# Performance work log

Hardware: AMD Instinct MI355X
Metric: run time of the kernel (lower is better)

Reference implementation:

```python
import math
import jax, jax.numpy as jnp
import numpy as np

E = 300
VOCAB = 50000
NUM_CLASSES = 34
ATTN_H = 150
B, S = 64, 2048


def setup_inputs() -> dict:
    key = jax.random.key(0)
    k1, k2, k3, k4, k5 = jax.random.split(key, 5)
    return {
        "input_x": jax.random.randint(k1, (B, S), 0, VOCAB, dtype=jnp.int32),
        "embedding": jax.random.normal(k2, (VOCAB, E), dtype=jnp.float32),
        "query": jax.random.normal(k3, (1, E), dtype=jnp.float32) * 0.1,
        "W_attention": jax.random.normal(k4, (E, ATTN_H), dtype=jnp.float32) * (1.0 / math.sqrt(E)),
        "W_out": jax.random.normal(k5, (2 * E, NUM_CLASSES), dtype=jnp.float32) * (1.0 / math.sqrt(2 * E)),
        "b": jnp.full((NUM_CLASSES,), 0.1, dtype=jnp.float32),
    }


def reference(input_x, embedding, query, W_attention, W_out, b):
    # Embedding lookup: [B, S, E]
    kv = embedding[input_x]
    scale = 1.0 / math.sqrt(E)
    # Stage 1: single learned query attends over all tokens
    s1 = jnp.einsum('e,bse->bs', query[0], kv) * scale          # [B, S]
    a1 = jax.nn.softmax(s1, axis=-1)
    h1 = jnp.einsum('bs,bse->be', a1, kv)                        # [B, E]
    # Stage 2: project h1 and keys through W_attention (no sqrt scaling in original)
    q2 = h1 @ W_attention                                        # [B, 150]
    k2 = jnp.einsum('bse,eh->bsh', kv, W_attention)              # [B, S, 150]
    s2 = jnp.einsum('bh,bsh->bs', q2, k2)                        # [B, S]
    a2 = jax.nn.softmax(s2, axis=-1)
    h2 = jnp.einsum('bs,bse->be', a2, kv)                        # [B, E]
    h = jnp.concatenate([h1, h2], axis=-1)                       # [B, 2E]
    # Dropout with keep_prob=1.0 (eval) is identity
    scores = h @ W_out + b                                       # [B, num_classes]
    return scores
```

## Files before the change

### kernel.cpp

```cpp
#include <hip/hip_runtime.h>
#include <math.h>

#define B_  64
#define S_  2048
#define E_  300
#define H_  150
#define C_  34
#define CHUNK 128
#define NCHUNK (S_ / CHUNK)
#define WAVES 4

__global__ __launch_bounds__(256, 4) void attn_pass(
    const int* __restrict__ x, const float* __restrict__ emb,
    const float* __restrict__ qmat, int q_stride, float scale,
    float* __restrict__ h_part, float* __restrict__ m_part,
    float* __restrict__ l_part)
{
    const int b     = blockIdx.y;
    const int chunk = blockIdx.x;
    const int tid   = threadIdx.x;
    const int w     = tid >> 6;
    const int lane  = tid & 63;

    const float4* qp = (const float4*)(qmat + (size_t)b * q_stride);
    float4 q0 = qp[lane];
    float4 q1 = make_float4(0.f, 0.f, 0.f, 0.f);
    if (lane < 11) q1 = qp[64 + lane];
    q0.x *= scale; q0.y *= scale; q0.z *= scale; q0.w *= scale;
    q1.x *= scale; q1.y *= scale; q1.z *= scale; q1.w *= scale;

    const int base = b * S_ + chunk * CHUNK;
    int myidx = 0;
    if (lane < 32) myidx = x[base + w + 4 * lane];

    float  m = -INFINITY, l = 0.f;
    float4 a0 = make_float4(0.f, 0.f, 0.f, 0.f);
    float4 a1 = make_float4(0.f, 0.f, 0.f, 0.f);

    for (int g = 0; g < 8; ++g) {
        float4 r0[4], r1[4];
        #pragma unroll
        for (int t = 0; t < 4; ++t) {
            const int row = __shfl(myidx, 4 * g + t);
            const float4* rp = (const float4*)(emb + (size_t)row * E_);
            r0[t] = rp[lane];
            r1[t] = make_float4(0.f, 0.f, 0.f, 0.f);
            if (lane < 11) r1[t] = rp[64 + lane];
        }
        float d[4];
        #pragma unroll
        for (int t = 0; t < 4; ++t)
            d[t] = q0.x * r0[t].x + q0.y * r0[t].y + q0.z * r0[t].z + q0.w * r0[t].w
                 + q1.x * r1[t].x + q1.y * r1[t].y + q1.z * r1[t].z + q1.w * r1[t].w;
        #pragma unroll
        for (int off = 32; off > 0; off >>= 1) {
            #pragma unroll
            for (int t = 0; t < 4; ++t) d[t] += __shfl_xor(d[t], off);
        }
        const float gm = fmaxf(fmaxf(d[0], d[1]), fmaxf(d[2], d[3]));
        const float mn = fmaxf(m, gm);
        const float c  = __expf(m - mn);
        const float p0 = __expf(d[0] - mn), p1 = __expf(d[1] - mn);
        const float p2 = __expf(d[2] - mn), p3 = __expf(d[3] - mn);
        l = l * c + ((p0 + p1) + (p2 + p3));
        a0.x = a0.x * c + p0 * r0[0].x + p1 * r0[1].x + p2 * r0[2].x + p3 * r0[3].x;
        a0.y = a0.y * c + p0 * r0[0].y + p1 * r0[1].y + p2 * r0[2].y + p3 * r0[3].y;
        a0.z = a0.z * c + p0 * r0[0].z + p1 * r0[1].z + p2 * r0[2].z + p3 * r0[3].z;
        a0.w = a0.w * c + p0 * r0[0].w + p1 * r0[1].w + p2 * r0[2].w + p3 * r0[3].w;
        a1.x = a1.x * c + p0 * r1[0].x + p1 * r1[1].x + p2 * r1[2].x + p3 * r1[3].x;
        a1.y = a1.y * c + p0 * r1[0].y + p1 * r1[1].y + p2 * r1[2].y + p3 * r1[3].y;
        a1.z = a1.z * c + p0 * r1[0].z + p1 * r1[1].z + p2 * r1[2].z + p3 * r1[3].z;
        a1.w = a1.w * c + p0 * r1[0].w + p1 * r1[1].w + p2 * r1[2].w + p3 * r1[3].w;
        m = mn;
    }

    __shared__ float sm[WAVES], sl[WAVES];
    __shared__ __align__(16) float sacc[WAVES][304];
    ((float4*)sacc[w])[lane] = a0;
    if (lane < 11) ((float4*)sacc[w])[64 + lane] = a1;
    if (lane == 0) { sm[w] = m; sl[w] = l; }
    __syncthreads();

    const float mb = fmaxf(fmaxf(sm[0], sm[1]), fmaxf(sm[2], sm[3]));
    const int pi = b * NCHUNK + chunk;
    for (int j = tid; j < E_; j += 256) {
        float h = 0.f;
        #pragma unroll
        for (int c = 0; c < WAVES; ++c)
            h += __expf(sm[c] - mb) * sacc[c][j];
        h_part[(size_t)pi * E_ + j] = h;
    }
    if (tid == 0) {
        float lb = 0.f;
        #pragma unroll
        for (int c = 0; c < WAVES; ++c) lb += __expf(sm[c] - mb) * sl[c];
        m_part[pi] = mb; l_part[pi] = lb;
    }
}

__global__ __launch_bounds__(320) void combine_qv(
    const float* __restrict__ h_part, const float* __restrict__ m_part,
    const float* __restrict__ l_part, const float* __restrict__ W,
    float* __restrict__ h1out, float* __restrict__ v2out)
{
    const int b = blockIdx.x, tid = threadIdx.x;
    __shared__ float sm[NCHUNK], sl[NCHUNK], sh[E_], sq[H_];
    if (tid < NCHUNK) { sm[tid] = m_part[b * NCHUNK + tid];
                        sl[tid] = l_part[b * NCHUNK + tid]; }
    __syncthreads();
    if (tid < E_) {
        float M = -INFINITY;
        #pragma unroll
        for (int c = 0; c < NCHUNK; ++c) M = fmaxf(M, sm[c]);
        float L = 0.f, h = 0.f;
        #pragma unroll
        for (int c = 0; c < NCHUNK; ++c) {
            const float wc = __expf(sm[c] - M);
            L += wc * sl[c];
            h += wc * h_part[((size_t)b * NCHUNK + c) * E_ + tid];
        }
        const float v = h / L;
        sh[tid] = v;
        h1out[b * E_ + tid] = v;
    }
    __syncthreads();
    if (tid < H_) {
        float acc = 0.f;
        for (int e = 0; e < E_; ++e) acc += sh[e] * W[e * H_ + tid];
        sq[tid] = acc;
    }
    __syncthreads();
    if (tid < E_) {
        float acc = 0.f;
        const float* wr = W + (size_t)tid * H_;
        for (int h = 0; h < H_; ++h) acc += sq[h] * wr[h];
        v2out[b * E_ + tid] = acc;
    }
}

__global__ __launch_bounds__(320) void combine_scores(
    const float* __restrict__ h_part, const float* __restrict__ m_part,
    const float* __restrict__ l_part, const float* __restrict__ h1,
    const float* __restrict__ Wout, const float* __restrict__ bias,
    float* __restrict__ out)
{
    const int b = blockIdx.x, tid = threadIdx.x;
    const int w = tid >> 6, lane = tid & 63;
    __shared__ float sm[NCHUNK], sl[NCHUNK];
    __shared__ float hh[2 * E_];
    if (tid < NCHUNK) { sm[tid] = m_part[b * NCHUNK + tid];
                        sl[tid] = l_part[b * NCHUNK + tid]; }
    if (tid < E_) hh[tid] = h1[b * E_ + tid];
    __syncthreads();
    if (tid < E_) {
        float M = -INFINITY;
        #pragma unroll
        for (int c = 0; c < NCHUNK; ++c) M = fmaxf(M, sm[c]);
        float L = 0.f, h = 0.f;
        #pragma unroll
        for (int c = 0; c < NCHUNK; ++c) {
            const float wc = __expf(sm[c] - M);
            L += wc * sl[c];
            h += wc * h_part[((size_t)b * NCHUNK + c) * E_ + tid];
        }
        hh[E_ + tid] = h / L;
    }
    __syncthreads();
    for (int c = w; c < C_; c += 5) {
        float p = 0.f;
        for (int e = lane; e < 2 * E_; e += 64)
            p += hh[e] * Wout[(size_t)e * C_ + c];
        #pragma unroll
        for (int off = 32; off > 0; off >>= 1) p += __shfl_xor(p, off);
        if (lane == 0) out[b * C_ + c] = p + bias[c];
    }
}

extern "C" void kernel_launch(void* const* d_in, const int* in_sizes, int n_in,
                              void* d_out, int out_size, void* d_ws, size_t ws_size,
                              hipStream_t stream) {
    const int*   x     = (const int*)  d_in[0];
    const float* emb   = (const float*)d_in[1];
    const float* query = (const float*)d_in[2];
    const float* Watt  = (const float*)d_in[3];
    const float* Wout  = (const float*)d_in[4];
    const float* bias  = (const float*)d_in[5];
    float* out = (float*)d_out;

    float* ws     = (float*)d_ws;
    float* h_part = ws;
    float* m_part = h_part + (size_t)B_ * NCHUNK * E_;
    float* l_part = m_part + B_ * NCHUNK;
    float* h1     = l_part + B_ * NCHUNK;
    float* v2     = h1 + B_ * E_;

    const float scale1 = 1.0f / sqrtf((float)E_);
    dim3 grid(NCHUNK, B_), blk(256);

    attn_pass<<<grid, blk, 0, stream>>>(x, emb, query, 0, scale1,
                                        h_part, m_part, l_part);
    combine_qv<<<B_, 320, 0, stream>>>(h_part, m_part, l_part, Watt, h1, v2);
    attn_pass<<<grid, blk, 0, stream>>>(x, emb, v2, E_, 1.0f,
                                        h_part, m_part, l_part);
    combine_scores<<<B_, 320, 0, stream>>>(h_part, m_part, l_part, h1,
                                           Wout, bias, out);
}
```

Before: 169.9 us.

## Fuse four kernel launches into one cooperative kernel with grid syncs

Replaces the four separate launches (two attention passes and two combine kernels) with a single cooperative kernel that uses grid-wide syncs between stages. Only chunk 0 of each batch row does the combine and projection work. This is meant to remove launch overhead and inter-kernel gaps. In exchange, the grid of 1024 blocks must be co-resident, the combine stages run on few blocks while others idle at the barrier, and grid.sync has its own cost. A fallback to the old launches is kept if the cooperative launch fails.

```diff
diff --git a/kernel.cpp b/kernel.cpp
--- a/kernel.cpp
+++ b/kernel.cpp
@@ -1,5 +1,8 @@
 #include <hip/hip_runtime.h>
+#include <hip/hip_cooperative_groups.h>
 #include <math.h>
+
+namespace cg = cooperative_groups;
 
 #define B_  64
 #define S_  2048
@@ -10,17 +13,15 @@
 #define NCHUNK (S_ / CHUNK)
 #define WAVES 4
 
-__global__ __launch_bounds__(256, 4) void attn_pass(
+__device__ __forceinline__ void attn_chunk(
     const int* __restrict__ x, const float* __restrict__ emb,
     const float* __restrict__ qmat, int q_stride, float scale,
     float* __restrict__ h_part, float* __restrict__ m_part,
-    float* __restrict__ l_part)
-{
-    const int b     = blockIdx.y;
-    const int chunk = blockIdx.x;
-    const int tid   = threadIdx.x;
-    const int w     = tid >> 6;
-    const int lane  = tid & 63;
+    float* __restrict__ l_part, int b, int chunk, int tid,
+    float* sm, float* sl, float (*sacc)[304])
+{
+    const int w    = tid >> 6;
+    const int lane = tid & 63;
 
     const float4* qp = (const float4*)(qmat + (size_t)b * q_stride);
     float4 q0 = qp[lane];
@@ -74,8 +75,6 @@
         m = mn;
     }
 
-    __shared__ float sm[WAVES], sl[WAVES];
-    __shared__ __align__(16) float sacc[WAVES][304];
     ((float4*)sacc[w])[lane] = a0;
     if (lane < 11) ((float4*)sacc[w])[64 + lane] = a1;
     if (lane == 0) { sm[w] = m; sl[w] = l; }
@@ -86,16 +85,124 @@
     for (int j = tid; j < E_; j += 256) {
         float h = 0.f;
         #pragma unroll
-        for (int c = 0; c < WAVES; ++c)
-            h += __expf(sm[c] - mb) * sacc[c][j];
+        for (int c2 = 0; c2 < WAVES; ++c2)
+            h += __expf(sm[c2] - mb) * sacc[c2][j];
         h_part[(size_t)pi * E_ + j] = h;
     }
     if (tid == 0) {
         float lb = 0.f;
         #pragma unroll
-        for (int c = 0; c < WAVES; ++c) lb += __expf(sm[c] - mb) * sl[c];
+        for (int c2 = 0; c2 < WAVES; ++c2) lb += __expf(sm[c2] - mb) * sl[c2];
         m_part[pi] = mb; l_part[pi] = lb;
     }
+    __syncthreads();
+}
+
+__global__ __launch_bounds__(256, 4) void fused(
+    const int* __restrict__ x, const float* __restrict__ emb,
+    const float* __restrict__ query, const float* __restrict__ Watt,
+    const float* __restrict__ Wout, const float* __restrict__ bias,
+    float* __restrict__ out,
+    float* __restrict__ h_part, float* __restrict__ m_part,
+    float* __restrict__ l_part, float* __restrict__ h1,
+    float* __restrict__ v2)
+{
+    const int chunk = blockIdx.x, b = blockIdx.y, tid = threadIdx.x;
+    cg::grid_group grid = cg::this_grid();
+
+    __shared__ float sm4[WAVES], sl4[WAVES];
+    __shared__ __align__(16) float sacc[WAVES][304];
+    __shared__ float smc[NCHUNK], slc[NCHUNK];
+    __shared__ float sh[E_];
+    __shared__ float sq[H_];
+    __shared__ float hh[2 * E_];
+
+    const float scale1 = 0.0577350269189626f;
+
+    attn_chunk(x, emb, query, 0, scale1, h_part, m_part, l_part,
+               b, chunk, tid, sm4, sl4, sacc);
+    grid.sync();
+
+    if (chunk == 0) {
+        if (tid < NCHUNK) { smc[tid] = m_part[b * NCHUNK + tid];
+                            slc[tid] = l_part[b * NCHUNK + tid]; }
+        __syncthreads();
+        float M = -INFINITY;
+        #pragma unroll
+        for (int c = 0; c < NCHUNK; ++c) M = fmaxf(M, smc[c]);
+        float L = 0.f;
+        #pragma unroll
+        for (int c = 0; c < NCHUNK; ++c) L += __expf(smc[c] - M) * slc[c];
+        for (int j = tid; j < E_; j += 256) {
+            float h = 0.f;
+            #pragma unroll
+            for (int c = 0; c < NCHUNK; ++c)
+                h += __expf(smc[c] - M) * h_part[((size_t)b * NCHUNK + c) * E_ + j];
+            const float v = h / L;
+            sh[j] = v;
+            h1[b * E_ + j] = v;
+        }
+        __syncthreads();
+        if (tid < H_) {
+            float acc = 0.f;
+            for (int e = 0; e < E_; ++e) acc += sh[e] * Watt[e * H_ + tid];
+            sq[tid] = acc;
+        }
+        __syncthreads();
+        for (int j = tid; j < E_; j += 256) {
+            float acc = 0.f;
+            const float* wr = Watt + (size_t)j * H_;
+            for (int h = 0; h < H_; ++h) acc += sq[h] * wr[h];
+            v2[b * E_ + j] = acc;
+        }
+    }
+    grid.sync();
+
+    attn_chunk(x, emb, v2, E_, 1.0f, h_part, m_part, l_part,
+               b, chunk, tid, sm4, sl4, sacc);
+    grid.sync();
+
+    if (chunk == 0) {
+        if (tid < NCHUNK) { smc[tid] = m_part[b * NCHUNK + tid];
+                            slc[tid] = l_part[b * NCHUNK + tid]; }
+        for (int j = tid; j < E_; j += 256) hh[j] = h1[b * E_ + j];
+        __syncthreads();
+        float M = -INFINITY;
+        #pragma unroll
+        for (int c = 0; c < NCHUNK; ++c) M = fmaxf(M, smc[c]);
+        float L = 0.f;
+        #pragma unroll
+        for (int c = 0; c < NCHUNK; ++c) L += __expf(smc[c] - M) * slc[c];
+        for (int j = tid; j < E_; j += 256) {
+            float h = 0.f;
+            #pragma unroll
+            for (int c = 0; c < NCHUNK; ++c)
+                h += __expf(smc[c] - M) * h_part[((size_t)b * NCHUNK + c) * E_ + j];
+            hh[E_ + j] = h / L;
+        }
+        __syncthreads();
+        const int w = tid >> 6, lane = tid & 63;
+        for (int c = w; c < C_; c += 4) {
+            float p = 0.f;
+            for (int e = lane; e < 2 * E_; e += 64)
+                p += hh[e] * Wout[(size_t)e * C_ + c];
+            #pragma unroll
+            for (int off = 32; off > 0; off >>= 1) p += __shfl_xor(p, off);
+            if (lane == 0) out[b * C_ + c] = p + bias[c];
+        }
+    }
+}
+
+__global__ __launch_bounds__(256, 4) void attn_pass(
+    const int* __restrict__ x, const float* __restrict__ emb,
+    const float* __restrict__ qmat, int q_stride, float scale,
+    float* __restrict__ h_part, float* __restrict__ m_part,
+    float* __restrict__ l_part)
+{
+    __shared__ float sm[WAVES], sl[WAVES];
+    __shared__ __align__(16) float sacc[WAVES][304];
+    attn_chunk(x, emb, qmat, q_stride, scale, h_part, m_part, l_part,
+               blockIdx.y, blockIdx.x, threadIdx.x, sm, sl, sacc);
 }
 
 __global__ __launch_bounds__(320) void combine_qv(
@@ -194,14 +301,23 @@
     float* h1     = l_part + B_ * NCHUNK;
     float* v2     = h1 + B_ * E_;
 
-    const float scale1 = 1.0f / sqrtf((float)E_);
     dim3 grid(NCHUNK, B_), blk(256);
 
-    attn_pass<<<grid, blk, 0, stream>>>(x, emb, query, 0, scale1,
-                                        h_part, m_part, l_part);
-    combine_qv<<<B_, 320, 0, stream>>>(h_part, m_part, l_part, Watt, h1, v2);
-    attn_pass<<<grid, blk, 0, stream>>>(x, emb, v2, E_, 1.0f,
-                                        h_part, m_part, l_part);
-    combine_scores<<<B_, 320, 0, stream>>>(h_part, m_part, l_part, h1,
-                                           Wout, bias, out);
-}
+    void* args[] = {
+        (void*)&x, (void*)&emb, (void*)&query, (void*)&Watt, (void*)&Wout,
+        (void*)&bias, (void*)&out, (void*)&h_part, (void*)&m_part,
+        (void*)&l_part, (void*)&h1, (void*)&v2
+    };
+    hipError_t err = hipLaunchCooperativeKernel((const void*)fused, grid, blk,
+                                                args, 0, stream);
+    if (err != hipSuccess) {
+        const float scale1 = 1.0f / sqrtf((float)E_);
+        attn_pass<<<grid, blk, 0, stream>>>(x, emb, query, 0, scale1,
+                                            h_part, m_part, l_part);
+        combine_qv<<<B_, 320, 0, stream>>>(h_part, m_part, l_part, Watt, h1, v2);
+        attn_pass<<<grid, blk, 0, stream>>>(x, emb, v2, E_, 1.0f,
+                                            h_part, m_part, l_part);
+        combine_scores<<<B_, 320, 0, stream>>>(h_part, m_part, l_part, h1,
+                                               Wout, bias, out);
+    }
+}
```

Result: slower. 518.0 us (+204.9%).

## Fuse combine kernels into attention passes via last-block atomic fan-in

Applied to the files above, without the earlier changes.

Each attention pass now ends with an atomic counter per batch row, and the last chunk block to finish does the cross-chunk softmax combine plus the following projection, instead of separate combine kernels. This drops two kernel launches and their inter-kernel gaps in exchange for a memset, atomics and threadfences. The combine work is now done by 256-thread blocks at the tail of the grid, which may serialize a little at the end.

```diff
diff --git a/kernel.cpp b/kernel.cpp
--- a/kernel.cpp
+++ b/kernel.cpp
@@ -10,17 +10,14 @@
 #define NCHUNK (S_ / CHUNK)
 #define WAVES 4
 
-__global__ __launch_bounds__(256, 4) void attn_pass(
+__device__ __forceinline__ void attn_chunk(
     const int* __restrict__ x, const float* __restrict__ emb,
     const float* __restrict__ qmat, int q_stride, float scale,
     float* __restrict__ h_part, float* __restrict__ m_part,
-    float* __restrict__ l_part)
-{
-    const int b     = blockIdx.y;
-    const int chunk = blockIdx.x;
-    const int tid   = threadIdx.x;
-    const int w     = tid >> 6;
-    const int lane  = tid & 63;
+    float* __restrict__ l_part, int b, int chunk, int tid)
+{
+    const int w    = tid >> 6;
+    const int lane = tid & 63;
 
     const float4* qp = (const float4*)(qmat + (size_t)b * q_stride);
     float4 q0 = qp[lane];
@@ -98,30 +95,50 @@
     }
 }
 
-__global__ __launch_bounds__(320) void combine_qv(
-    const float* __restrict__ h_part, const float* __restrict__ m_part,
-    const float* __restrict__ l_part, const float* __restrict__ W,
-    float* __restrict__ h1out, float* __restrict__ v2out)
-{
-    const int b = blockIdx.x, tid = threadIdx.x;
-    __shared__ float sm[NCHUNK], sl[NCHUNK], sh[E_], sq[H_];
-    if (tid < NCHUNK) { sm[tid] = m_part[b * NCHUNK + tid];
-                        sl[tid] = l_part[b * NCHUNK + tid]; }
-    __syncthreads();
-    if (tid < E_) {
-        float M = -INFINITY;
-        #pragma unroll
-        for (int c = 0; c < NCHUNK; ++c) M = fmaxf(M, sm[c]);
-        float L = 0.f, h = 0.f;
-        #pragma unroll
-        for (int c = 0; c < NCHUNK; ++c) {
-            const float wc = __expf(sm[c] - M);
-            L += wc * sl[c];
-            h += wc * h_part[((size_t)b * NCHUNK + c) * E_ + tid];
-        }
+__device__ __forceinline__ bool fanin_last(int* cnt, int b, int tid)
+{
+    __shared__ int lastFlag;
+    __threadfence();
+    if (tid == 0)
+        lastFlag = (atomicAdd(&cnt[b], 1) == NCHUNK - 1);
+    __syncthreads();
+    if (!lastFlag) return false;
+    __threadfence();
+    return true;
+}
+
+__global__ __launch_bounds__(256, 4) void attn1_qv(
+    const int* __restrict__ x, const float* __restrict__ emb,
+    const float* __restrict__ query, const float* __restrict__ W,
+    float* __restrict__ h_part, float* __restrict__ m_part,
+    float* __restrict__ l_part, float* __restrict__ h1,
+    float* __restrict__ v2, int* __restrict__ cnt)
+{
+    const int b = blockIdx.y, chunk = blockIdx.x, tid = threadIdx.x;
+    const float scale1 = 0.05773502691896258f;
+
+    attn_chunk(x, emb, query, 0, scale1, h_part, m_part, l_part, b, chunk, tid);
+
+    if (!fanin_last(cnt, b, tid)) return;
+
+    __shared__ float smc[NCHUNK], slc[NCHUNK], sh[E_], sq[H_];
+    if (tid < NCHUNK) { smc[tid] = m_part[b * NCHUNK + tid];
+                        slc[tid] = l_part[b * NCHUNK + tid]; }
+    __syncthreads();
+    float M = -INFINITY;
+    #pragma unroll
+    for (int c = 0; c < NCHUNK; ++c) M = fmaxf(M, smc[c]);
+    float L = 0.f;
+    #pragma unroll
+    for (int c = 0; c < NCHUNK; ++c) L += __expf(smc[c] - M) * slc[c];
+    for (int j = tid; j < E_; j += 256) {
+        float h = 0.f;
+        #pragma unroll
+        for (int c = 0; c < NCHUNK; ++c)
+            h += __expf(smc[c] - M) * h_part[((size_t)b * NCHUNK + c) * E_ + j];
         const float v = h / L;
-        sh[tid] = v;
-        h1out[b * E_ + tid] = v;
+        sh[j] = v;
+        h1[b * E_ + j] = v;
     }
     __syncthreads();
     if (tid < H_) {
@@ -130,43 +147,50 @@
         sq[tid] = acc;
     }
     __syncthreads();
-    if (tid < E_) {
+    for (int j = tid; j < E_; j += 256) {
         float acc = 0.f;
-        const float* wr = W + (size_t)tid * H_;
+        const float* wr = W + (size_t)j * H_;
         for (int h = 0; h < H_; ++h) acc += sq[h] * wr[h];
-        v2out[b * E_ + tid] = acc;
-    }
-}
-
-__global__ __launch_bounds__(320) void combine_scores(
-    const float* __restrict__ h_part, const float* __restrict__ m_part,
-    const float* __restrict__ l_part, const float* __restrict__ h1,
+        v2[b * E_ + j] = acc;
+    }
+}
+
+__global__ __launch_bounds__(256, 4) void attn2_scores(
+    const int* __restrict__ x, const float* __restrict__ emb,
+    const float* __restrict__ v2, const float* __restrict__ h1,
     const float* __restrict__ Wout, const float* __restrict__ bias,
-    float* __restrict__ out)
-{
-    const int b = blockIdx.x, tid = threadIdx.x;
+    float* __restrict__ h_part, float* __restrict__ m_part,
+    float* __restrict__ l_part, float* __restrict__ out,
+    int* __restrict__ cnt)
+{
+    const int b = blockIdx.y, chunk = blockIdx.x, tid = threadIdx.x;
+
+    attn_chunk(x, emb, v2, E_, 1.0f, h_part, m_part, l_part, b, chunk, tid);
+
+    if (!fanin_last(cnt, b, tid)) return;
+
+    __shared__ float smc[NCHUNK], slc[NCHUNK];
+    __shared__ float hh[2 * E_];
+    if (tid < NCHUNK) { smc[tid] = m_part[b * NCHUNK + tid];
+                        slc[tid] = l_part[b * NCHUNK + tid]; }
+    for (int j = tid; j < E_; j += 256) hh[j] = h1[b * E_ + j];
+    __syncthreads();
+    float M = -INFINITY;
+    #pragma unroll
+    for (int c = 0; c < NCHUNK; ++c) M = fmaxf(M, smc[c]);
+    float L = 0.f;
+    #pragma unroll
+    for (int c = 0; c < NCHUNK; ++c) L += __expf(smc[c] - M) * slc[c];
+    for (int j = tid; j < E_; j += 256) {
+        float h = 0.f;
+        #pragma unroll
+        for (int c = 0; c < NCHUNK; ++c)
+            h += __expf(smc[c] - M) * h_part[((size_t)b * NCHUNK + c) * E_ + j];
+        hh[E_ + j] = h / L;
+    }
+    __syncthreads();
     const int w = tid >> 6, lane = tid & 63;
-    __shared__ float sm[NCHUNK], sl[NCHUNK];
-    __shared__ float hh[2 * E_];
-    if (tid < NCHUNK) { sm[tid] = m_part[b * NCHUNK + tid];
-                        sl[tid] = l_part[b * NCHUNK + tid]; }
-    if (tid < E_) hh[tid] = h1[b * E_ + tid];
-    __syncthreads();
-    if (tid < E_) {
-        float M = -INFINITY;
-        #pragma unroll
-        for (int c = 0; c < NCHUNK; ++c) M = fmaxf(M, sm[c]);
-        float L = 0.f, h = 0.f;
-        #pragma unroll
-        for (int c = 0; c < NCHUNK; ++c) {
-            const float wc = __expf(sm[c] - M);
-            L += wc * sl[c];
-            h += wc * h_part[((size_t)b * NCHUNK + c) * E_ + tid];
-        }
-        hh[E_ + tid] = h / L;
-    }
-    __syncthreads();
-    for (int c = w; c < C_; c += 5) {
+    for (int c = w; c < C_; c += 4) {
         float p = 0.f;
         for (int e = lane; e < 2 * E_; e += 64)
             p += hh[e] * Wout[(size_t)e * C_ + c];
@@ -193,15 +217,14 @@
     float* l_part = m_part + B_ * NCHUNK;
     float* h1     = l_part + B_ * NCHUNK;
     float* v2     = h1 + B_ * E_;
-
-    const float scale1 = 1.0f / sqrtf((float)E_);
+    int*   cnt1   = (int*)(v2 + B_ * E_);
+    int*   cnt2   = cnt1 + B_;
+
+    hipMemsetAsync(cnt1, 0, 2 * B_ * sizeof(int), stream);
+
     dim3 grid(NCHUNK, B_), blk(256);
-
-    attn_pass<<<grid, blk, 0, stream>>>(x, emb, query, 0, scale1,
-                                        h_part, m_part, l_part);
-    combine_qv<<<B_, 320, 0, stream>>>(h_part, m_part, l_part, Watt, h1, v2);
-    attn_pass<<<grid, blk, 0, stream>>>(x, emb, v2, E_, 1.0f,
-                                        h_part, m_part, l_part);
-    combine_scores<<<B_, 320, 0, stream>>>(h_part, m_part, l_part, h1,
-                                           Wout, bias, out);
-}
+    attn1_qv<<<grid, blk, 0, stream>>>(x, emb, query, Watt,
+                                       h_part, m_part, l_part, h1, v2, cnt1);
+    attn2_scores<<<grid, blk, 0, stream>>>(x, emb, v2, h1, Wout, bias,
+                                           h_part, m_part, l_part, out, cnt2);
+}
```

Measured after the change: 442.7 us. 2.61x slower.
